# Kernel tuning notes

Hardware: AMD Instinct MI355X
Metric: run time of the kernel (lower is better)

Reference implementation:

```python
import jax, jax.numpy as jnp
import numpy as np

B, C, H, W = 8, 256, 128, 128
WS = 8   # window size
NH = 8   # num heads
NEG = -1e9


def _rel_coords_table(ws):
    # continuous relative coords table, shape [1, 2ws-1, 2ws-1, 2]
    r = np.arange(-(ws - 1), ws, dtype=np.float32)
    t = np.stack(np.meshgrid(r, r, indexing='ij'), axis=-1)[None]
    t = t / (ws - 1) * 8.0
    t = np.sign(t) * np.log2(np.abs(t) + 1.0) / np.log2(8.0)
    return jnp.asarray(t, dtype=jnp.float32)


def _rel_pos_index(ws):
    coords = np.stack(np.meshgrid(np.arange(ws), np.arange(ws), indexing='ij'))  # [2,ws,ws]
    flat = coords.reshape(2, -1)
    rel = (flat[:, :, None] - flat[:, None, :]).transpose(1, 2, 0).astype(np.int64)  # [N,N,2]
    rel[..., 0] += ws - 1
    rel[..., 1] += ws - 1
    rel[..., 0] *= 2 * ws - 1
    return jnp.asarray(rel.sum(-1))  # [N,N]


def setup_inputs() -> dict:
    key = jax.random.key(0)
    ks = jax.random.split(key, 10)
    d8 = C // 8
    return {
        'x': jax.random.normal(ks[0], (B, C, H, W), jnp.float32),
        'y': jax.random.normal(ks[1], (B, C, H, W), jnp.float32),
        'Wq': jax.random.normal(ks[2], (d8, C), jnp.float32) * 0.02,
        'bq': jnp.zeros((d8,), jnp.float32),
        'Wk': jax.random.normal(ks[3], (d8, C), jnp.float32) * 0.02,
        'bk': jnp.zeros((d8,), jnp.float32),
        'Wv': jax.random.normal(ks[4], (C, C), jnp.float32) * 0.02,
        'bv': jnp.zeros((C,), jnp.float32),
        'gamma': jnp.full((1,), 0.5, jnp.float32),
        'qkv_w': jax.random.normal(ks[5], (3 * C, C), jnp.float32) * 0.02,
        'q_bias': jnp.zeros((C,), jnp.float32),
        'v_bias': jnp.zeros((C,), jnp.float32),
        'logit_scale': jnp.log(10.0 * jnp.ones((NH, 1, 1), jnp.float32)),
        'cpb_w1': jax.random.normal(ks[6], (512, 2), jnp.float32) * 0.02,
        'cpb_b1': jnp.zeros((512,), jnp.float32),
        'cpb_w2': jax.random.normal(ks[7], (NH, 512), jnp.float32) * 0.02,
        'proj_w': jax.random.normal(ks[8], (C, C), jnp.float32) * 0.02,
        'proj_b': jnp.zeros((C,), jnp.float32),
    }


def _criss_cross(x, y, Wq, bq, Wk, bk, Wv, bv, gamma):
    # 1x1 convs as einsum channel projections
    q = jnp.einsum('bchw,oc->bohw', x, Wq) + bq[None, :, None, None]
    k = jnp.einsum('bchw,oc->bohw', x, Wk) + bk[None, :, None, None]
    v = jnp.einsum('bchw,oc->bohw', y, Wv) + bv[None, :, None, None]
    h = x.shape[2]
    # column (H-axis) attention with -inf on diagonal; row (W-axis) attention
    diag = jnp.where(jnp.eye(h, dtype=bool), NEG, 0.0).astype(x.dtype)  # [H,H]
    eH = jnp.einsum('bchw,bcgw->bhwg', q, k) + diag[None, :, None, :]   # [B,H,W,H]
    eW = jnp.einsum('bchw,bchv->bhwv', q, k)                            # [B,H,W,W]
    att = jax.nn.softmax(jnp.concatenate([eH, eW], axis=3), axis=3)
    aH, aW = att[..., :h], att[..., h:]
    oH = jnp.einsum('bhwg,bcgw->bchw', aH, v)
    oW = jnp.einsum('bhwv,bchv->bchw', aW, v)
    return gamma[0] * (oH + oW) + x


def _window_attention(xw, qkv_w, q_bias, v_bias, logit_scale,
                      cpb_w1, cpb_b1, cpb_w2, proj_w, proj_b):
    B_, N, Cc = xw.shape
    hd = Cc // NH
    bias = jnp.concatenate([q_bias, jnp.zeros_like(v_bias), v_bias])
    qkv = (xw @ qkv_w.T + bias).reshape(B_, N, 3, NH, hd).transpose(2, 0, 3, 1, 4)
    q, k, v = qkv[0], qkv[1], qkv[2]  # [B_, NH, N, hd]
    qn = q / jnp.maximum(jnp.linalg.norm(q, axis=-1, keepdims=True), 1e-12)
    kn = k / jnp.maximum(jnp.linalg.norm(k, axis=-1, keepdims=True), 1e-12)
    scale = jnp.exp(jnp.minimum(logit_scale, jnp.log(jnp.float32(100.0))))  # [NH,1,1]
    attn = jnp.einsum('bhnd,bhmd->bhnm', qn, kn) * scale[None]
    # continuous relative position bias via inline MLP
    tbl = jax.nn.relu(_rel_coords_table(WS) @ cpb_w1.T + cpb_b1) @ cpb_w2.T  # [1,2ws-1,2ws-1,NH]
    tbl = tbl.reshape(-1, NH)
    rpb = tbl[_rel_pos_index(WS).reshape(-1)].reshape(N, N, NH).transpose(2, 0, 1)
    attn = jax.nn.softmax(attn + (16.0 * jax.nn.sigmoid(rpb))[None], axis=-1)
    out = jnp.einsum('bhnm,bhmd->bnhd', attn, v).reshape(B_, N, Cc)
    return out @ proj_w.T + proj_b


def reference(x, y, Wq, bq, Wk, bk, Wv, bv, gamma,
              qkv_w, q_bias, v_bias, logit_scale,
              cpb_w1, cpb_b1, cpb_w2, proj_w, proj_b):
    cc = _criss_cross(x, y, Wq, bq, Wk, bk, Wv, bv, gamma)   # [B,C,H,W]
    xh = cc.transpose(0, 2, 3, 1)                            # [B,H,W,C]
    win = xh.reshape(B, H // WS, WS, W // WS, WS, C)
    win = win.transpose(0, 1, 3, 2, 4, 5).reshape(-1, WS * WS, C)
    wa = _window_attention(win, qkv_w, q_bias, v_bias, logit_scale,
                           cpb_w1, cpb_b1, cpb_w2, proj_w, proj_b)
    out = wa.reshape(B, H // WS, W // WS, WS, WS, C)
    out = out.transpose(0, 1, 3, 2, 4, 5).reshape(B, H, W, C)
    return out.transpose(0, 3, 1, 2)                         # [B,C,H,W]
```

## Files before the change

kernel.cpp:

```cpp
#include <hip/hip_runtime.h>
#include <cstdio>
#include <cstddef>
#include <cstdint>

#define F_B 8
#define F_C 256
#define F_H 128
#define F_W 128
#define F_HW 16384

typedef __attribute__((ext_vector_type(8))) short short8;
typedef __attribute__((ext_vector_type(4))) short short4v;
typedef __attribute__((ext_vector_type(4))) float float4v;

__device__ __forceinline__ unsigned short f2bf(float f) {
  union {
    float f;
    uint32_t u;
  } v;
  v.f = f;
  return (unsigned short)((v.u + 0x7fffu + ((v.u >> 16) & 1u)) >> 16);
}

__device__ __forceinline__ float bf2f(unsigned short u) {
  union {
    uint32_t u;
    float f;
  } v;
  v.u = ((uint32_t)u) << 16;
  return v.f;
}

__device__ __forceinline__ void async_copy16(const unsigned short* g, unsigned short* l) {
  __builtin_amdgcn_global_load_lds((const __attribute__((address_space(1))) void*)g,
                                   (__attribute__((address_space(3))) void*)l, 16, 0, 0);
}

__global__ void build_aux2(const float* __restrict__ Wq, const float* __restrict__ Wk,
                           const float* __restrict__ bq, const float* __restrict__ bk,
                           const float* __restrict__ q_bias, const float* __restrict__ v_bias,
                           const float* __restrict__ Wv, const float* __restrict__ qkv_w,
                           const float* __restrict__ proj_w, unsigned short* __restrict__ qk_wb,
                           float* __restrict__ qk_b, float* __restrict__ qkv_b,
                           unsigned short* __restrict__ Wvb, unsigned short* __restrict__ qkv_wb,
                           unsigned short* __restrict__ proj_wb) {
  int t = blockIdx.x * 256 + threadIdx.x;
  if (t < 8192) {
    qk_wb[t] = f2bf(Wq[t]);
    qk_wb[8192 + t] = f2bf(Wk[t]);
  }
  if (t < 65536) {
    Wvb[t] = f2bf(Wv[t]);
    proj_wb[t] = f2bf(proj_w[t]);
  }
  if (t < 196608) qkv_wb[t] = f2bf(qkv_w[t]);
  if (t < 32) {
    qk_b[t] = bq[t];
    qk_b[32 + t] = bk[t];
  }
  if (t < 256) {
    qkv_b[t] = q_bias[t];
    qkv_b[256 + t] = 0.0f;
    qkv_b[512 + t] = v_bias[t];
  }
}

__device__ __forceinline__ float cpb_coord(int a) {
  float v = (float)(a - 7) * (8.0f / 7.0f);
  float lg = log2f(fabsf(v) + 1.0f) * (1.0f / 3.0f);
  return (v < 0.0f) ? -lg : lg;
}

__global__ void cpb_table(const float* __restrict__ w1, const float* __restrict__ b1,
                          const float* __restrict__ w2, float* __restrict__ tblS) {
  int e = blockIdx.x;
  int yi = e / 15, xi = e % 15;
  float ry = cpb_coord(yi), rx = cpb_coord(xi);
  __shared__ float hid[512];
  int t = threadIdx.x;
  for (int j = t; j < 512; j += 256) {
    float hv = w1[j * 2] * ry + w1[j * 2 + 1] * rx + b1[j];
    hid[j] = fmaxf(hv, 0.0f);
  }
  __syncthreads();
  if (t < 8) {
    float s = 0.0f;
    for (int j = 0; j < 512; j++) s += hid[j] * w2[t * 512 + j];
    tblS[e * 8 + t] = 16.0f / (1.0f + __expf(-s));
  }
}

__global__ void build_rpbt(const float* __restrict__ tblS, float* __restrict__ rpbt) {
  int t = blockIdx.x * 256 + threadIdx.x;
  int h = t >> 12, i = (t >> 6) & 63, j = t & 63;
  int e = ((i >> 3) - (j >> 3) + 7) * 15 + ((i & 7) - (j & 7) + 7);
  rpbt[t] = tblS[e * 8 + h];
}

__global__ void transpose_bf(const float* __restrict__ in, unsigned short* __restrict__ outb) {
  __shared__ float tile[32][33];
  int b = blockIdx.z;
  int p0 = blockIdx.x * 32;
  int c0 = blockIdx.y * 32;
  const float* src = in + (size_t)b * F_C * F_HW;
  int t = threadIdx.x;
  int tx = t & 31, ty = t >> 5;
#pragma unroll
  for (int i = 0; i < 4; i++) {
    tile[ty + i * 8][tx] = src[(size_t)(c0 + ty + i * 8) * F_HW + p0 + tx];
  }
  __syncthreads();
  int pix = t >> 3, cl = (t & 7) * 4;
  short4v pk;
#pragma unroll
  for (int u = 0; u < 4; u++) pk[u] = (short)f2bf(tile[cl + u][pix]);
  size_t idx = (size_t)b * F_HW * F_C + (size_t)(p0 + pix) * F_C + c0 + cl;
  *(short4v*)(outb + idx) = pk;
}

template <int BN, int OUT>
__global__ __launch_bounds__(256) void gemm_mfma(const unsigned short* __restrict__ A,
                                                 const unsigned short* __restrict__ Wt,
                                                 const float* __restrict__ bias, void* Cmat,
                                                 int M, int N, int gx) {
  constexpr int WN = BN / 2;
  constexpr int NREP = WN / 16;
  __shared__ __align__(16) unsigned short As[128 * 32];
  __shared__ __align__(16) unsigned short Bs[BN * 32];
  int nwg = gridDim.x;
  int id = blockIdx.x;
  int cpx = nwg >> 3;
  int swz = (id & 7) * cpx + (id >> 3);
  int by = swz / gx;
  int bx = swz - by * gx;
  int m0 = by * 128;
  int n0 = bx * BN;
  int t = threadIdx.x;
  int wid = t >> 6, lane = t & 63;
  int wr = wid >> 1, wc = wid & 1;

  float4v acc[4][NREP] = {};

  for (int k0 = 0; k0 < 256; k0 += 32) {
    __syncthreads();
#pragma unroll
    for (int j = 0; j < 2; j++) {
      int r = wid * 32 + j * 16 + (lane >> 2);
      int kg = (lane & 3) ^ ((r >> 1) & 3);
      const unsigned short* gp = A + (size_t)(m0 + r) * 256 + k0 + kg * 8;
      async_copy16(gp, As + (wid * 32 + j * 16) * 32);
    }
#pragma unroll
    for (int j = 0; j < BN / 64; j++) {
      int r = wid * (BN / 4) + j * 16 + (lane >> 2);
      int kg = (lane & 3) ^ ((r >> 1) & 3);
      const unsigned short* gp = Wt + (size_t)(n0 + r) * 256 + k0 + kg * 8;
      async_copy16(gp, Bs + (wid * (BN / 4) + j * 16) * 32);
    }
    __syncthreads();
    short8 af[4];
#pragma unroll
    for (int mi = 0; mi < 4; mi++) {
      int row = wr * 64 + mi * 16 + (lane & 15);
      int kg = (lane >> 4) ^ ((row >> 1) & 3);
      af[mi] = *(const short8*)(As + row * 32 + kg * 8);
    }
    short8 bfr[NREP];
#pragma unroll
    for (int ni = 0; ni < NREP; ni++) {
      int col = wc * WN + ni * 16 + (lane & 15);
      int kg = (lane >> 4) ^ ((col >> 1) & 3);
      bfr[ni] = *(const short8*)(Bs + col * 32 + kg * 8);
    }
#pragma unroll
    for (int mi = 0; mi < 4; mi++)
#pragma unroll
      for (int ni = 0; ni < NREP; ni++) {
        if (OUT != 1)
          acc[mi][ni] =
              __builtin_amdgcn_mfma_f32_16x16x32_bf16(bfr[ni], af[mi], acc[mi][ni], 0, 0, 0);
        else
          acc[mi][ni] =
              __builtin_amdgcn_mfma_f32_16x16x32_bf16(af[mi], bfr[ni], acc[mi][ni], 0, 0, 0);
      }
  }
  if (OUT != 1) {
#pragma unroll
    for (int mi = 0; mi < 4; mi++) {
      int row = m0 + wr * 64 + mi * 16 + (lane & 15);
#pragma unroll
      for (int ni = 0; ni < NREP; ni++) {
        int col0 = n0 + wc * WN + ni * 16 + (lane >> 4) * 4;
        float4 bn = *(const float4*)(bias + col0);
        float v0 = acc[mi][ni][0] + bn.x;
        float v1 = acc[mi][ni][1] + bn.y;
        float v2 = acc[mi][ni][2] + bn.z;
        float v3 = acc[mi][ni][3] + bn.w;
        if (OUT == 0) {
          float4 st = {v0, v1, v2, v3};
          *(float4*)((float*)Cmat + (size_t)row * N + col0) = st;
        } else {
          short4v pk;
          pk[0] = (short)f2bf(v0);
          pk[1] = (short)f2bf(v1);
          pk[2] = (short)f2bf(v2);
          pk[3] = (short)f2bf(v3);
          *(short4v*)((unsigned short*)Cmat + (size_t)row * N + col0) = pk;
        }
      }
    }
  } else {
#pragma unroll
    for (int ni = 0; ni < NREP; ni++) {
      int col = n0 + wc * WN + ni * 16 + (lane & 15);
      float bn = bias[col];
#pragma unroll
      for (int mi = 0; mi < 4; mi++) {
        int row0 = m0 + wr * 64 + mi * 16 + (lane >> 4) * 4;
        float4 st;
        st.x = acc[mi][ni][0] + bn;
        st.y = acc[mi][ni][1] + bn;
        st.z = acc[mi][ni][2] + bn;
        st.w = acc[mi][ni][3] + bn;
        int bb = row0 >> 14, p = row0 & 16383;
        *(float4*)((float*)Cmat + ((size_t)bb * N + col) * F_HW + p) = st;
      }
    }
  }
}

template <int MODE>
__global__ __launch_bounds__(256) void cc_logits(const float* __restrict__ qk,
                                                 unsigned short* __restrict__ e,
                                                 float* __restrict__ sums) {
  int x = blockIdx.x;
  int b = blockIdx.y;
  size_t base = (size_t)b * F_HW;
  __shared__ float kt[32][132];
  int t = threadIdx.x;
  {
    int gk = t >> 1, c0 = (t & 1) * 16;
    size_t krow = (MODE == 0) ? ((size_t)gk * F_W + x) : ((size_t)x * F_W + gk);
    const float4* src = (const float4*)(qk + (base + krow) * 64 + 32 + c0);
#pragma unroll
    for (int q4 = 0; q4 < 4; q4++) {
      float4 v = src[q4];
      kt[c0 + q4 * 4 + 0][gk] = v.x;
      kt[c0 + q4 * 4 + 1][gk] = v.y;
      kt[c0 + q4 * 4 + 2][gk] = v.z;
      kt[c0 + q4 * 4 + 3][gk] = v.w;
    }
  }
  __syncthreads();
  int i = t >> 1, g0 = (t & 1) * 64;
  size_t qrow = (MODE == 0) ? ((size_t)i * F_W + x) : ((size_t)x * F_W + i);
  const float4* qp = (const float4*)(qk + (base + qrow) * 64);
  float qreg[32];
#pragma unroll
  for (int q4 = 0; q4 < 8; q4++) {
    float4 v = qp[q4];
    qreg[q4 * 4 + 0] = v.x;
    qreg[q4 * 4 + 1] = v.y;
    qreg[q4 * 4 + 2] = v.z;
    qreg[q4 * 4 + 3] = v.w;
  }
  float acc[64];
#pragma unroll
  for (int g = 0; g < 64; g++) acc[g] = 0.0f;
  for (int c = 0; c < 32; c++) {
    float qv = qreg[c];
#pragma unroll
    for (int g = 0; g < 64; g++) acc[g] += qv * kt[c][g0 + g];
  }
  if (MODE == 0) {
    int d = i - g0;
    if (d >= 0 && d < 64) acc[d] = -1e9f;
  }
  unsigned short* ep = e + (base + qrow) * 256 + MODE * 128 + g0;
  float s = 0.0f;
#pragma unroll
  for (int g = 0; g < 64; g += 8) {
    short8 pk;
#pragma unroll
    for (int j = 0; j < 8; j++) {
      float ev = __expf(acc[g + j]);
      s += ev;
      pk[j] = (short)f2bf(ev);
    }
    *(short8*)(ep + g) = pk;
  }
  s += __shfl_xor(s, 1);
  if ((t & 1) == 0) sums[base + qrow] = s;
}

template <int MODE>
__global__ __launch_bounds__(256) void cc_pv_mfma(const unsigned short* __restrict__ eb,
                                                  const unsigned short* __restrict__ vtb,
                                                  const float* __restrict__ sumH,
                                                  const float* __restrict__ sumW,
                                                  const float* __restrict__ gamma,
                                                  const unsigned short* __restrict__ xb,
                                                  unsigned short* __restrict__ pob,
                                                  unsigned short* __restrict__ ccb) {
  int x = blockIdx.x, b = blockIdx.y;
  size_t base = (size_t)b * F_HW;
  __shared__ __align__(16) unsigned short As[128 * 128];
  __shared__ __align__(16) unsigned short Vs[256 * 64];
  int t = threadIdx.x;
  int wid = t >> 6, lane = t & 63;
  int wr = wid >> 1, wc = wid & 1;
  {
    int i = t >> 1, half = t & 1;
    size_t pix = (MODE == 0) ? ((size_t)i * F_W + x) : ((size_t)x * F_W + i);
    float rv = 1.0f / (sumH[base + pix] + sumW[base + pix]);
    const unsigned short* ep = eb + (base + pix) * 256 + MODE * 128 + half * 64;
    int g = ((i >> 3) & 7) ^ (i & 7);
#pragma unroll
    for (int s = 0; s < 8; s++) {
      short8 vin = *(const short8*)(ep + s * 8);
      short8 vo;
#pragma unroll
      for (int j = 0; j < 8; j++) vo[j] = (short)f2bf(bf2f((unsigned short)vin[j]) * rv);
      int slot = (half * 8 + s) ^ g;
      *(short8*)(As + i * 128 + slot * 8) = vo;
    }
  }
  float4v acc[4][8] = {};
#pragma unroll
  for (int kc = 0; kc < 2; kc++) {
    __syncthreads();
    {
      int ko = t >> 5, cj = t & 31;
      short8 rowv[8];
#pragma unroll
      for (int r = 0; r < 8; r++) {
        int kk = kc * 64 + ko * 8 + r;
        size_t pixk = (MODE == 0) ? ((size_t)kk * F_W + x) : ((size_t)x * F_W + kk);
        rowv[r] = *(const short8*)(vtb + (base + pixk) * 256 + cj * 8);
      }
#pragma unroll
      for (int j = 0; j < 8; j++) {
        short8 col;
#pragma unroll
        for (int r = 0; r < 8; r++) col[r] = rowv[r][j];
        int c = cj * 8 + j;
        int slot = ko ^ ((c >> 3) & 7) ^ (c & 7);
        *(short8*)(Vs + c * 64 + slot * 8) = col;
      }
    }
    __syncthreads();
#pragma unroll
    for (int ksub = 0; ksub < 2; ksub++) {
      short8 af[4];
#pragma unroll
      for (int mi = 0; mi < 4; mi++) {
        int i = wr * 64 + mi * 16 + (lane & 15);
        int slot = (kc * 8 + ksub * 4 + (lane >> 4)) ^ ((i >> 3) & 7) ^ (i & 7);
        af[mi] = *(const short8*)(As + i * 128 + slot * 8);
      }
      short8 bfv[8];
#pragma unroll
      for (int ni = 0; ni < 8; ni++) {
        int c = wc * 128 + ni * 16 + (lane & 15);
        int slot = (ksub * 4 + (lane >> 4)) ^ ((c >> 3) & 7) ^ (c & 7);
        bfv[ni] = *(const short8*)(Vs + c * 64 + slot * 8);
      }
#pragma unroll
      for (int mi = 0; mi < 4; mi++)
#pragma unroll
        for (int ni = 0; ni < 8; ni++)
          acc[mi][ni] =
              __builtin_amdgcn_mfma_f32_16x16x32_bf16(bfv[ni], af[mi], acc[mi][ni], 0, 0, 0);
    }
  }
  float gm = gamma[0];
#pragma unroll
  for (int mi = 0; mi < 4; mi++) {
    int i = wr * 64 + mi * 16 + (lane & 15);
    size_t pix = (MODE == 0) ? ((size_t)i * F_W + x) : ((size_t)x * F_W + i);
    size_t rowb = (base + pix) * 256;
#pragma unroll
    for (int ni = 0; ni < 8; ni++) {
      int c0 = wc * 128 + ni * 16 + (lane >> 4) * 4;
      if (MODE == 0) {
        short4v pk;
#pragma unroll
        for (int r = 0; r < 4; r++) pk[r] = (short)f2bf(acc[mi][ni][r]);
        *(short4v*)(pob + rowb + c0) = pk;
      } else {
        short4v po4 = *(const short4v*)(pob + rowb + c0);
        short4v xb4 = *(const short4v*)(xb + rowb + c0);
        short4v pk;
#pragma unroll
        for (int r = 0; r < 4; r++)
          pk[r] = (short)f2bf(gm * (bf2f((unsigned short)po4[r]) + acc[mi][ni][r]) +
                              bf2f((unsigned short)xb4[r]));
        *(short4v*)(ccb + rowb + c0) = pk;
      }
    }
  }
}

__global__ __launch_bounds__(256) void win_attn_mfma(const unsigned short* __restrict__ qkv,
                                                     const float* __restrict__ logit_scale,
                                                     const float* __restrict__ rpbt,
                                                     unsigned short* __restrict__ out) {
  __shared__ __align__(16) unsigned short Pl[4][4096];
  __shared__ __align__(16) unsigned short Vt[4][2048];
  int win = blockIdx.x;
  int wid = threadIdx.x >> 6, lane = threadIdx.x & 63;
  int hh = blockIdx.y * 4 + wid;
  int b = win >> 8, wy = (win >> 4) & 15, wx = win & 15;
  size_t pbase = (size_t)b * F_HW + (size_t)(wy * 8) * F_W + wx * 8;
  int il = lane & 15, kg = lane >> 4;

  short8 qb[4], ka[4];
#pragma unroll
  for (int ni = 0; ni < 4; ni++) {
    int i = ni * 16 + il;
    size_t row = (pbase + (size_t)(i >> 3) * F_W + (i & 7)) * 768 + hh * 32 + kg * 8;
    short8 qv = *(const short8*)(qkv + row);
    short8 kv = *(const short8*)(qkv + row + 256);
    float qss = 0.0f, kss = 0.0f;
#pragma unroll
    for (int j = 0; j < 8; j++) {
      float qf = bf2f((unsigned short)qv[j]);
      float kf = bf2f((unsigned short)kv[j]);
      qss += qf * qf;
      kss += kf * kf;
    }
    qss += __shfl_xor(qss, 16);
    qss += __shfl_xor(qss, 32);
    kss += __shfl_xor(kss, 16);
    kss += __shfl_xor(kss, 32);
    float qinv = 1.0f / fmaxf(sqrtf(qss), 1e-12f);
    float kinv = 1.0f / fmaxf(sqrtf(kss), 1e-12f);
#pragma unroll
    for (int j = 0; j < 8; j++) {
      qb[ni][j] = (short)f2bf(bf2f((unsigned short)qv[j]) * qinv);
      ka[ni][j] = (short)f2bf(bf2f((unsigned short)kv[j]) * kinv);
    }
  }

  if (lane < 32) {
    int jb = lane >> 2, db = lane & 3;
    short8 rows[8];
#pragma unroll
    for (int r = 0; r < 8; r++) {
      rows[r] =
          *(const short8*)(qkv + (pbase + (size_t)jb * F_W + r) * 768 + hh * 32 + 512 + db * 8);
    }
#pragma unroll
    for (int c = 0; c < 8; c++) {
      int d = db * 8 + c;
      short8 col;
#pragma unroll
      for (int r = 0; r < 8; r++) col[r] = rows[r][c];
      *(short8*)(Vt[wid] + d * 64 + ((jb ^ (d & 7)) * 8)) = col;
    }
  }

  float4v sacc[4][4] = {};
#pragma unroll
  for (int mj = 0; mj < 4; mj++)
#pragma unroll
    for (int ni = 0; ni < 4; ni++)
      sacc[mj][ni] = __builtin_amdgcn_mfma_f32_16x16x32_bf16(ka[mj], qb[ni], sacc[mj][ni], 0, 0, 0);

  float scale = __expf(fminf(logit_scale[hh], 4.605170185988091f));

#pragma unroll
  for (int ni = 0; ni < 4; ni++) {
    int i = ni * 16 + il;
    const float* rp = rpbt + ((size_t)hh * 64 + i) * 64;
    float sv[16];
    float mx = -1e30f;
#pragma unroll
    for (int mj = 0; mj < 4; mj++) {
      float4 rb = *(const float4*)(rp + mj * 16 + kg * 4);
      float rbs[4] = {rb.x, rb.y, rb.z, rb.w};
#pragma unroll
      for (int r = 0; r < 4; r++) {
        float v = sacc[mj][ni][r] * scale + rbs[r];
        sv[mj * 4 + r] = v;
        mx = fmaxf(mx, v);
      }
    }
    mx = fmaxf(mx, __shfl_xor(mx, 16));
    mx = fmaxf(mx, __shfl_xor(mx, 32));
    float sm = 0.0f;
#pragma unroll
    for (int u = 0; u < 16; u++) {
      sv[u] = __expf(sv[u] - mx);
      sm += sv[u];
    }
    sm += __shfl_xor(sm, 16);
    sm += __shfl_xor(sm, 32);
    float inv = 1.0f / sm;
#pragma unroll
    for (int mj = 0; mj < 4; mj++) {
      int j0 = mj * 16 + kg * 4;
      short4v pk;
#pragma unroll
      for (int r = 0; r < 4; r++) pk[r] = (short)f2bf(sv[mj * 4 + r] * inv);
      int byteoff = i * 128 + (((j0 >> 3) ^ (i & 7)) * 16) + (j0 & 7) * 2;
      *(short4v*)((char*)Pl[wid] + byteoff) = pk;
    }
  }
  __syncthreads();

  float4v oacc[2][4] = {};
#pragma unroll
  for (int kc = 0; kc < 2; kc++) {
    short8 va[2];
#pragma unroll
    for (int md = 0; md < 2; md++) {
      int d = md * 16 + il;
      va[md] = *(const short8*)((char*)Vt[wid] + d * 128 + (((kc * 4 + kg) ^ (d & 7)) * 16));
    }
    short8 pb[4];
#pragma unroll
    for (int ni = 0; ni < 4; ni++) {
      int i = ni * 16 + il;
      pb[ni] = *(const short8*)((char*)Pl[wid] + i * 128 + (((kc * 4 + kg) ^ (i & 7)) * 16));
    }
#pragma unroll
    for (int md = 0; md < 2; md++)
#pragma unroll
      for (int ni = 0; ni < 4; ni++)
        oacc[md][ni] =
            __builtin_amdgcn_mfma_f32_16x16x32_bf16(va[md], pb[ni], oacc[md][ni], 0, 0, 0);
  }

#pragma unroll
  for (int ni = 0; ni < 4; ni++) {
    int i = ni * 16 + il;
    size_t orow = (pbase + (size_t)(i >> 3) * F_W + (i & 7)) * 256 + hh * 32;
#pragma unroll
    for (int md = 0; md < 2; md++) {
      int d0 = md * 16 + kg * 4;
      short4v pk;
#pragma unroll
      for (int r = 0; r < 4; r++) pk[r] = (short)f2bf(oacc[md][ni][r]);
      *(short4v*)(out + orow + d0) = pk;
    }
  }
}

extern "C" void kernel_launch(void* const* d_in, const int* in_sizes, int n_in,
                              void* d_out, int out_size, void* d_ws, size_t ws_size,
                              hipStream_t stream) {
  const float* x = (const float*)d_in[0];
  const float* y = (const float*)d_in[1];
  const float* Wq = (const float*)d_in[2];
  const float* bq = (const float*)d_in[3];
  const float* Wk = (const float*)d_in[4];
  const float* bk = (const float*)d_in[5];
  const float* Wv = (const float*)d_in[6];
  const float* bv = (const float*)d_in[7];
  const float* gamma = (const float*)d_in[8];
  const float* qkv_w = (const float*)d_in[9];
  const float* q_bias = (const float*)d_in[10];
  const float* v_bias = (const float*)d_in[11];
  const float* logit_scale = (const float*)d_in[12];
  const float* cpb_w1 = (const float*)d_in[13];
  const float* cpb_b1 = (const float*)d_in[14];
  const float* cpb_w2 = (const float*)d_in[15];
  const float* proj_w = (const float*)d_in[16];
  const float* proj_b = (const float*)d_in[17];

  float* ws = (float*)d_ws;
  const size_t NPX = (size_t)F_B * F_HW;
  const size_t M1 = NPX * 256;
  size_t f_xb = 0;
  size_t f_ytb = M1 / 2;
  size_t f_vtb = M1;
  size_t f_pob = M1 + M1 / 2;
  size_t f_ccb = 2 * M1;
  size_t f_qkb = 2 * M1 + M1 / 2;
  size_t f_wts = f_qkb + NPX * 64;
  size_t o_qkwb = f_wts;
  size_t o_Wvb = o_qkwb + 8192;
  size_t o_qkvwb = o_Wvb + 32768;
  size_t o_projwb = o_qkvwb + 98304;
  size_t o_qkb2 = o_projwb + 32768;
  size_t o_qkvb2 = o_qkb2 + 64;
  size_t o_tbl = o_qkvb2 + 768;
  size_t o_sumH = o_tbl + 1800;
  size_t o_sumW = o_sumH + NPX;
  size_t o_rpbt = o_sumW + NPX;
  size_t need = (o_rpbt + 32768) * sizeof(float);
  if (ws_size < need) {
    fprintf(stderr, "kernel_launch: ws too small: %zu < %zu\n", ws_size, need);
    return;
  }
  unsigned short* xb = (unsigned short*)(ws + f_xb);
  unsigned short* qkvb = (unsigned short*)(ws + f_xb);
  unsigned short* ytb = (unsigned short*)(ws + f_ytb);
  unsigned short* eb = (unsigned short*)(ws + f_ytb);
  unsigned short* vtb = (unsigned short*)(ws + f_vtb);
  unsigned short* pob = (unsigned short*)(ws + f_pob);
  unsigned short* attn_b = (unsigned short*)(ws + f_pob);
  unsigned short* ccb = (unsigned short*)(ws + f_ccb);
  float* qkb = ws + f_qkb;
  unsigned short* qk_wb = (unsigned short*)(ws + o_qkwb);
  unsigned short* Wvb = (unsigned short*)(ws + o_Wvb);
  unsigned short* qkv_wb = (unsigned short*)(ws + o_qkvwb);
  unsigned short* proj_wb = (unsigned short*)(ws + o_projwb);
  float* qk_b = ws + o_qkb2;
  float* qkv_b = ws + o_qkvb2;
  float* tblS = ws + o_tbl;
  float* sumH = ws + o_sumH;
  float* sumW = ws + o_sumW;
  float* rpbt = ws + o_rpbt;

  build_aux2<<<dim3(768), dim3(256), 0, stream>>>(Wq, Wk, bq, bk, q_bias, v_bias, Wv, qkv_w,
                                                  proj_w, qk_wb, qk_b, qkv_b, Wvb, qkv_wb,
                                                  proj_wb);
  cpb_table<<<dim3(225), dim3(256), 0, stream>>>(cpb_w1, cpb_b1, cpb_w2, tblS);
  build_rpbt<<<dim3(128), dim3(256), 0, stream>>>(tblS, rpbt);
  transpose_bf<<<dim3(512, 8, 8), dim3(256), 0, stream>>>(x, xb);
  transpose_bf<<<dim3(512, 8, 8), dim3(256), 0, stream>>>(y, ytb);
  gemm_mfma<64, 0><<<dim3(1024), dim3(256), 0, stream>>>(xb, qk_wb, qk_b, qkb, (int)NPX, 64,
                                                         1);
  gemm_mfma<128, 2><<<dim3(2048), dim3(256), 0, stream>>>(ytb, Wvb, bv, vtb, (int)NPX, 256, 2);
  cc_logits<0><<<dim3(128, 8), dim3(256), 0, stream>>>(qkb, eb, sumH);
  cc_logits<1><<<dim3(128, 8), dim3(256), 0, stream>>>(qkb, eb, sumW);
  cc_pv_mfma<0><<<dim3(128, 8), dim3(256), 0, stream>>>(eb, vtb, sumH, sumW, gamma, xb, pob,
                                                        ccb);
  cc_pv_mfma<1><<<dim3(128, 8), dim3(256), 0, stream>>>(eb, vtb, sumH, sumW, gamma, xb, pob,
                                                        ccb);
  gemm_mfma<128, 2><<<dim3(6144), dim3(256), 0, stream>>>(ccb, qkv_wb, qkv_b, qkvb, (int)NPX,
                                                          768, 6);
  win_attn_mfma<<<dim3(2048, 2), dim3(256), 0, stream>>>(qkvb, logit_scale, rpbt, attn_b);
  gemm_mfma<128, 1><<<dim3(2048), dim3(256), 0, stream>>>(attn_b, proj_wb, proj_b, d_out,
                                                          (int)NPX, 256, 2);
}
```

Measured before the change: 654.5 us.

## Double-buffer LDS tiles in MFMA GEMM and unify epilogue orientation

The GEMM now keeps two LDS buffers for A and B and issues the async copy of the next K slice before computing on the current one, with one barrier per iteration instead of two. This is meant to hide global-load latency behind the MFMA work. The MFMA operand order is also unified so every output mode uses the transposed accumulator layout. For the OUT 0 and OUT 2 modes that means scalar, column-strided stores in place of vectorized row stores, which may cost store efficiency. LDS use doubles, which could lower occupancy.

```diff
diff --git a/kernel.cpp b/kernel.cpp
--- a/kernel.cpp
+++ b/kernel.cpp
@@ -125,8 +125,8 @@
                                                  int M, int N, int gx) {
   constexpr int WN = BN / 2;
   constexpr int NREP = WN / 16;
-  __shared__ __align__(16) unsigned short As[128 * 32];
-  __shared__ __align__(16) unsigned short Bs[BN * 32];
+  __shared__ __align__(16) unsigned short As[2][128 * 32];
+  __shared__ __align__(16) unsigned short Bs[2][BN * 32];
   int nwg = gridDim.x;
   int id = blockIdx.x;
   int cpx = nwg >> 3;
@@ -139,84 +139,61 @@
   int wid = t >> 6, lane = t & 63;
   int wr = wid >> 1, wc = wid & 1;
 
+  int rA = wid * 32 + (lane >> 2);
+  int kgA = (lane & 3) ^ ((rA >> 1) & 3);
+  const unsigned short* gpA = A + (size_t)(m0 + rA) * 256 + kgA * 8;
+  int rB = wid * (BN / 4) + (lane >> 2);
+  int kgB = (lane & 3) ^ ((rB >> 1) & 3);
+  const unsigned short* gpB = Wt + (size_t)(n0 + rB) * 256 + kgB * 8;
+
+  auto STAGE = [&](int buf, int k0) {
+#pragma unroll
+    for (int j = 0; j < 2; j++)
+      async_copy16(gpA + (size_t)j * 16 * 256 + k0, &As[buf][(wid * 32 + j * 16) * 32]);
+#pragma unroll
+    for (int j = 0; j < BN / 64; j++)
+      async_copy16(gpB + (size_t)j * 16 * 256 + k0,
+                   &Bs[buf][(wid * (BN / 4) + j * 16) * 32]);
+  };
+
   float4v acc[4][NREP] = {};
 
+  STAGE(0, 0);
+  __syncthreads();
+  int cur = 0;
   for (int k0 = 0; k0 < 256; k0 += 32) {
-    __syncthreads();
-#pragma unroll
-    for (int j = 0; j < 2; j++) {
-      int r = wid * 32 + j * 16 + (lane >> 2);
-      int kg = (lane & 3) ^ ((r >> 1) & 3);
-      const unsigned short* gp = A + (size_t)(m0 + r) * 256 + k0 + kg * 8;
-      async_copy16(gp, As + (wid * 32 + j * 16) * 32);
-    }
-#pragma unroll
-    for (int j = 0; j < BN / 64; j++) {
-      int r = wid * (BN / 4) + j * 16 + (lane >> 2);
-      int kg = (lane & 3) ^ ((r >> 1) & 3);
-      const unsigned short* gp = Wt + (size_t)(n0 + r) * 256 + k0 + kg * 8;
-      async_copy16(gp, Bs + (wid * (BN / 4) + j * 16) * 32);
-    }
-    __syncthreads();
+    if (k0 < 224) STAGE(cur ^ 1, k0 + 32);
     short8 af[4];
 #pragma unroll
     for (int mi = 0; mi < 4; mi++) {
       int row = wr * 64 + mi * 16 + (lane & 15);
       int kg = (lane >> 4) ^ ((row >> 1) & 3);
-      af[mi] = *(const short8*)(As + row * 32 + kg * 8);
+      af[mi] = *(const short8*)(&As[cur][row * 32 + kg * 8]);
     }
     short8 bfr[NREP];
 #pragma unroll
     for (int ni = 0; ni < NREP; ni++) {
       int col = wc * WN + ni * 16 + (lane & 15);
       int kg = (lane >> 4) ^ ((col >> 1) & 3);
-      bfr[ni] = *(const short8*)(Bs + col * 32 + kg * 8);
+      bfr[ni] = *(const short8*)(&Bs[cur][col * 32 + kg * 8]);
     }
 #pragma unroll
     for (int mi = 0; mi < 4; mi++)
 #pragma unroll
-      for (int ni = 0; ni < NREP; ni++) {
-        if (OUT != 1)
-          acc[mi][ni] =
-              __builtin_amdgcn_mfma_f32_16x16x32_bf16(bfr[ni], af[mi], acc[mi][ni], 0, 0, 0);
-        else
-          acc[mi][ni] =
-              __builtin_amdgcn_mfma_f32_16x16x32_bf16(af[mi], bfr[ni], acc[mi][ni], 0, 0, 0);
-      }
-  }
-  if (OUT != 1) {
+      for (int ni = 0; ni < NREP; ni++)
+        acc[mi][ni] =
+            __builtin_amdgcn_mfma_f32_16x16x32_bf16(af[mi], bfr[ni], acc[mi][ni], 0, 0, 0);
+    __syncthreads();
+    cur ^= 1;
+  }
+#pragma unroll
+  for (int ni = 0; ni < NREP; ni++) {
+    int col = n0 + wc * WN + ni * 16 + (lane & 15);
+    float bn = bias[col];
 #pragma unroll
     for (int mi = 0; mi < 4; mi++) {
-      int row = m0 + wr * 64 + mi * 16 + (lane & 15);
-#pragma unroll
-      for (int ni = 0; ni < NREP; ni++) {
-        int col0 = n0 + wc * WN + ni * 16 + (lane >> 4) * 4;
-        float4 bn = *(const float4*)(bias + col0);
-        float v0 = acc[mi][ni][0] + bn.x;
-        float v1 = acc[mi][ni][1] + bn.y;
-        float v2 = acc[mi][ni][2] + bn.z;
-        float v3 = acc[mi][ni][3] + bn.w;
-        if (OUT == 0) {
-          float4 st = {v0, v1, v2, v3};
-          *(float4*)((float*)Cmat + (size_t)row * N + col0) = st;
-        } else {
-          short4v pk;
-          pk[0] = (short)f2bf(v0);
-          pk[1] = (short)f2bf(v1);
-          pk[2] = (short)f2bf(v2);
-          pk[3] = (short)f2bf(v3);
-          *(short4v*)((unsigned short*)Cmat + (size_t)row * N + col0) = pk;
-        }
-      }
-    }
-  } else {
-#pragma unroll
-    for (int ni = 0; ni < NREP; ni++) {
-      int col = n0 + wc * WN + ni * 16 + (lane & 15);
-      float bn = bias[col];
-#pragma unroll
-      for (int mi = 0; mi < 4; mi++) {
-        int row0 = m0 + wr * 64 + mi * 16 + (lane >> 4) * 4;
+      int row0 = m0 + wr * 64 + mi * 16 + (lane >> 4) * 4;
+      if (OUT == 1) {
         float4 st;
         st.x = acc[mi][ni][0] + bn;
         st.y = acc[mi][ni][1] + bn;
@@ -224,6 +201,16 @@
         st.w = acc[mi][ni][3] + bn;
         int bb = row0 >> 14, p = row0 & 16383;
         *(float4*)((float*)Cmat + ((size_t)bb * N + col) * F_HW + p) = st;
+      } else {
+#pragma unroll
+        for (int r = 0; r < 4; r++) {
+          float v = acc[mi][ni][r] + bn;
+          int row = row0 + r;
+          if (OUT == 0)
+            ((float*)Cmat)[(size_t)row * N + col] = v;
+          else
+            ((unsigned short*)Cmat)[(size_t)row * N + col] = f2bf(v);
+        }
       }
     }
   }
```

Result: faster. 635.7 us (-2.9%).
